# Optimization experiments

Measured on AMD Instinct MI355X. Metric: run time of the kernel, lower is better.

## Reference

```python
import jax, jax.numpy as jnp
import numpy as np
from jax import lax

# BatchNorm2d(affine=False) in eval mode with initial running stats (mean=0, var=1)
# reduces to a constant scale. (Original torch module in train mode would use batch
# stats of the dispatched subset; we use the eval-mode form for a deterministic,
# vectorizable reference.)
BN_SCALE = 1.0 / np.sqrt(1.0 + 1e-5)
DN = ('NCHW', 'OIHW', 'NCHW')


def _dw(x, w, pad, dil=1):
    # depthwise conv, kernel [C,1,k,k]
    return lax.conv_general_dilated(x, w, (1, 1), [(pad, pad), (pad, pad)],
                                    rhs_dilation=(dil, dil), dimension_numbers=DN,
                                    feature_group_count=x.shape[1])


def _pw(x, w):
    # pointwise 1x1 conv, kernel [C,C,1,1]
    return lax.conv_general_dilated(x, w, (1, 1), 'VALID', dimension_numbers=DN)


def _sep(x, d1, p1, d2, p2, pad):
    # DARTS SepConv: (ReLU-dw-pw-BN) x 2
    y = _pw(_dw(jax.nn.relu(x), d1, pad), p1) * BN_SCALE
    return _pw(_dw(jax.nn.relu(y), d2, pad), p2) * BN_SCALE


def _dil(x, d, p, pad):
    # DARTS DilConv: ReLU-dw(dilation=2)-pw-BN
    return _pw(_dw(jax.nn.relu(x), d, pad, 2), p) * BN_SCALE


def _maxpool3(x):
    y = jnp.pad(x, ((0, 0), (0, 0), (1, 1), (1, 1)), constant_values=-jnp.inf)
    return lax.reduce_window(y, -jnp.inf, lax.max, (1, 1, 3, 3), (1, 1, 1, 1), 'VALID')


def _avgpool3(x):
    # avg_pool 3x3 stride 1 pad 1, count_include_pad=False
    pad = [(0, 0), (0, 0), (1, 1), (1, 1)]
    s = lax.reduce_window(x, 0.0, lax.add, (1, 1, 3, 3), (1, 1, 1, 1), pad)
    c = lax.reduce_window(jnp.ones_like(x), 0.0, lax.add, (1, 1, 3, 3), (1, 1, 1, 1), pad)
    return s / c


def _mixed_forward(x, weights, params, top):
    B, n_op = weights.shape
    _, idx = lax.top_k(weights, top)                    # [B, top]
    sel = jax.nn.one_hot(idx, n_op).sum(axis=1) > 0     # [B, n_op] bool: op in top-k
    # softmax over logits masked to -inf outside top-k => non-selected ops weight 0
    gate = jax.nn.softmax(jnp.where(sel, weights, -jnp.inf), axis=-1)  # [B, n_op]
    (sc3_d1, sc3_p1, sc3_d2, sc3_p2,
     sc5_d1, sc5_p1, sc5_d2, sc5_p2,
     dc3_d, dc3_p, dc5_d, dc5_p) = params
    # PRIMITIVES order: none, max_pool_3x3, avg_pool_3x3, skip_connect,
    # sep_conv_3x3, sep_conv_5x5, dil_conv_3x3, dil_conv_5x5
    op_outs = [
        None,                        # 'none' contributes zeros
        _maxpool3(x) * BN_SCALE,     # pool ops are followed by BN(affine=False)
        _avgpool3(x) * BN_SCALE,
        x,                           # skip_connect (stride=1 -> Identity)
        _sep(x, sc3_d1, sc3_p1, sc3_d2, sc3_p2, 1),
        _sep(x, sc5_d1, sc5_p1, sc5_d2, sc5_p2, 2),
        _dil(x, dc3_d, dc3_p, 2),
        _dil(x, dc5_d, dc5_p, 4),
    ]
    out = jnp.zeros_like(x)
    for i, y in enumerate(op_outs):
        if y is not None:
            out = out + gate[:, i, None, None, None] * y
    return out, weights  # second output is gate_value_cp (clone of gate input)


def setup_inputs():
    key = jax.random.key(0)
    ks = jax.random.split(key, 16)
    B, C, H, W = 64, 128, 32, 32
    def p(k, shape):
        return jax.random.normal(k, shape, jnp.float32) * 0.05
    return {
        'x': jax.random.normal(ks[0], (B, C, H, W), jnp.float32),
        'weights': jax.random.normal(ks[1], (B, 8), jnp.float32),
        'sc3_d1': p(ks[2], (C, 1, 3, 3)), 'sc3_p1': p(ks[3], (C, C, 1, 1)),
        'sc3_d2': p(ks[4], (C, 1, 3, 3)), 'sc3_p2': p(ks[5], (C, C, 1, 1)),
        'sc5_d1': p(ks[6], (C, 1, 5, 5)), 'sc5_p1': p(ks[7], (C, C, 1, 1)),
        'sc5_d2': p(ks[8], (C, 1, 5, 5)), 'sc5_p2': p(ks[9], (C, C, 1, 1)),
        'dc3_d': p(ks[10], (C, 1, 3, 3)), 'dc3_p': p(ks[11], (C, C, 1, 1)),
        'dc5_d': p(ks[12], (C, 1, 5, 5)), 'dc5_p': p(ks[13], (C, C, 1, 1)),
        'top': 2,
    }


def reference(x, weights, sc3_d1, sc3_p1, sc3_d2, sc3_p2, sc5_d1, sc5_p1, sc5_d2, sc5_p2, dc3_d, dc3_p, dc5_d, dc5_p, top):
    params = (sc3_d1, sc3_p1, sc3_d2, sc3_p2, sc5_d1, sc5_p1, sc5_d2, sc5_p2,
              dc3_d, dc3_p, dc5_d, dc5_p)
    return _mixed_forward(x, weights, params, top)
```

## Files before the change

### kernel.cpp

```cpp
#include <hip/hip_runtime.h>
#include <hip/hip_bf16.h>


#define BN_SCALE 0.9999950000374997f
#define BB 64
#define CC 128
#define HH 32
#define WW 32
#define PLANE (HH*WW)
#define SAMP (CC*PLANE)
#define NOUT0 (BB*SAMP)

typedef __attribute__((ext_vector_type(8))) short bf16x8;
typedef __attribute__((ext_vector_type(4))) float f32x4;

__device__ __forceinline__ float us2f(unsigned int u) {
    unsigned int x = (u & 0xffffu) << 16;
    float f; __builtin_memcpy(&f, &x, 4); return f;
}
__device__ __forceinline__ unsigned short f2us(float f) {
    __hip_bfloat16 h = __float2bfloat16(f);
    unsigned short u; __builtin_memcpy(&u, &h, 2); return u;
}

__global__ void k_gates(const float* __restrict__ wlog,
                        const void* __restrict__ topp,
                        float* __restrict__ gates,
                        int* __restrict__ cnum, int* __restrict__ cops,
                        float* __restrict__ out_w) {
    int b = threadIdx.x;

    int top = -1;
    {
        unsigned int u0 = *(const unsigned int*)topp;
        int i32 = (int)u0;
        if (i32 >= 1 && i32 <= 8) top = i32;
        else {
            float f32; __builtin_memcpy(&f32, &u0, 4);
            if (f32 >= 1.f && f32 <= 8.f) top = (int)(f32 + 0.5f);
            else { float fb = us2f(u0); if (fb >= 1.f && fb <= 8.f) top = (int)(fb + 0.5f); }
        }
        if (top < 1 || top > 8) top = 2;
    }

    float lw[8];
    #pragma unroll
    for (int i = 0; i < 8; ++i) {
        lw[i] = wlog[b * 8 + i];
        out_w[b * 8 + i] = lw[i];
    }
    bool sel[8] = {false,false,false,false,false,false,false,false};
    for (int t = 0; t < top; ++t) {
        int best = -1; float bv = -3.4e38f;
        #pragma unroll
        for (int i = 0; i < 8; ++i)
            if (!sel[i] && lw[i] > bv) { bv = lw[i]; best = i; }
        if (best >= 0) sel[best] = true;
    }
    float m = -3.4e38f;
    #pragma unroll
    for (int i = 0; i < 8; ++i) if (sel[i] && lw[i] > m) m = lw[i];
    float s = 0.f, e[8];
    #pragma unroll
    for (int i = 0; i < 8; ++i) { e[i] = sel[i] ? expf(lw[i] - m) : 0.f; s += e[i]; }
    float inv = (s > 0.f) ? 1.f / s : 0.f;
    float g[8];
    #pragma unroll
    for (int i = 0; i < 8; ++i) {
        g[i] = (s > 0.f) ? e[i] * inv : (sel[i] ? 1.f / (float)top : 0.f);
        gates[b * 8 + i] = g[i];
    }
    int n = 0;
    #pragma unroll
    for (int i = 4; i < 8; ++i)
        if (g[i] > 0.f) { if (n < 4) cops[b * 4 + n] = i; ++n; }
    cnum[b] = (n < 4) ? n : 4;
}

__global__ __launch_bounds__(256) void
k_prep(const float* __restrict__ w0, const float* __restrict__ w1,
       const float* __restrict__ w2, const float* __restrict__ w3,
       const float* __restrict__ w4, const float* __restrict__ w5,
       unsigned short* __restrict__ Wbf) {
    int idx = blockIdx.x * 256 + threadIdx.x;
    int mat = idx >> 14, e = idx & 16383;
    const float* src; float s = 1.f;
    switch (mat) {
        case 0:  src = w0; s = BN_SCALE; break;
        case 1:  src = w1; s = BN_SCALE; break;
        case 2:  src = w2; break;
        case 3:  src = w3; break;
        case 4:  src = w4; break;
        default: src = w5; break;
    }
    Wbf[idx] = f2us(src[e] * s);
}

__global__ __launch_bounds__(256) void
k_pools(const float* __restrict__ x,
        const float* __restrict__ gates,
        float* __restrict__ out) {
    int plane = blockIdx.x;
    int b = plane >> 7;
    float g1 = gates[b * 8 + 1] * BN_SCALE;
    float g2 = gates[b * 8 + 2] * BN_SCALE;
    float g3 = gates[b * 8 + 3];
    float* op = out + (size_t)plane * PLANE;
    if (g1 == 0.f && g2 == 0.f && g3 == 0.f) {
        ((float4*)op)[threadIdx.x] = make_float4(0.f, 0.f, 0.f, 0.f);
        return;
    }
    __shared__ float sx[PLANE];
    ((float4*)sx)[threadIdx.x] = ((const float4*)(x + (size_t)plane * PLANE))[threadIdx.x];
    __syncthreads();
    #pragma unroll
    for (int j = 0; j < 4; ++j) {
        int px = threadIdx.x + j * 256;
        int h = px >> 5, w = px & 31;
        float mx = -3.4e38f, sm = 0.f;
        int cnt = 0;
        #pragma unroll
        for (int dh = -1; dh <= 1; ++dh) {
            int ih = h + dh;
            if ((unsigned)ih >= HH) continue;
            #pragma unroll
            for (int dw = -1; dw <= 1; ++dw) {
                int iw = w + dw;
                if ((unsigned)iw >= WW) continue;
                float v = sx[ih * WW + iw];
                mx = fmaxf(mx, v);
                sm += v;
                ++cnt;
            }
        }
        op[px] = g1 * mx + g2 * (sm / (float)cnt) + g3 * sx[px];
    }
}

template <int K, int DIL>
__device__ __forceinline__ void dw_comp(const float* __restrict__ sx,
                                        const float* __restrict__ wd, int c,
                                        unsigned short* __restrict__ opp) {
    constexpr int PAD = (K / 2) * DIL;
    float wk[K * K];
    #pragma unroll
    for (int i = 0; i < K * K; ++i) wk[i] = wd[c * K * K + i];
    #pragma unroll
    for (int j = 0; j < 4; ++j) {
        int px = threadIdx.x + j * 256;
        int h = px >> 5, w = px & 31;
        float acc = 0.f;
        #pragma unroll
        for (int ky = 0; ky < K; ++ky) {
            int ih = h + ky * DIL - PAD;
            if ((unsigned)ih >= HH) continue;
            #pragma unroll
            for (int kx = 0; kx < K; ++kx) {
                int iw = w + kx * DIL - PAD;
                if ((unsigned)iw >= WW) continue;
                acc = fmaf(wk[ky * K + kx], sx[ih * WW + iw], acc);
            }
        }
        opp[px] = f2us(acc);
    }
}

__global__ __launch_bounds__(256) void
k_dw_first(const float* __restrict__ x,
           const float* __restrict__ w4, const float* __restrict__ w5,
           const float* __restrict__ w6, const float* __restrict__ w7,
           const float* __restrict__ gates,
           unsigned short* __restrict__ A4, unsigned short* __restrict__ A5,
           unsigned short* __restrict__ P6, unsigned short* __restrict__ P7) {
    int plane = blockIdx.x;
    int b = plane >> 7, c = plane & 127;
    float g4 = gates[b * 8 + 4], g5 = gates[b * 8 + 5];
    float g6 = gates[b * 8 + 6], g7 = gates[b * 8 + 7];
    if (g4 == 0.f && g5 == 0.f && g6 == 0.f && g7 == 0.f) return;
    __shared__ float sx[PLANE];
    {
        float4 v = ((const float4*)(x + (size_t)plane * PLANE))[threadIdx.x];
        ((float4*)sx)[threadIdx.x] =
            make_float4(fmaxf(v.x, 0.f), fmaxf(v.y, 0.f),
                        fmaxf(v.z, 0.f), fmaxf(v.w, 0.f));
    }
    __syncthreads();
    size_t off = (size_t)plane * PLANE;
    if (g4 != 0.f) dw_comp<3, 1>(sx, w4, c, A4 + off);
    if (g5 != 0.f) dw_comp<5, 1>(sx, w5, c, A5 + off);
    if (g6 != 0.f) dw_comp<3, 2>(sx, w6, c, P6 + off);
    if (g7 != 0.f) dw_comp<5, 2>(sx, w7, c, P7 + off);
}

__global__ __launch_bounds__(256) void
k_dw_second(const unsigned short* __restrict__ B4,
            const unsigned short* __restrict__ B5,
            const float* __restrict__ w4, const float* __restrict__ w5,
            const float* __restrict__ gates,
            unsigned short* __restrict__ P4, unsigned short* __restrict__ P5) {
    int plane = blockIdx.x;
    int b = plane >> 7, c = plane & 127;
    float g4 = gates[b * 8 + 4], g5 = gates[b * 8 + 5];
    if (g4 == 0.f && g5 == 0.f) return;
    __shared__ float sx[PLANE];
    size_t off = (size_t)plane * PLANE;
    if (g4 != 0.f) {
        ushort4 v = ((const ushort4*)(B4 + off))[threadIdx.x];
        ((float4*)sx)[threadIdx.x] =
            make_float4(fmaxf(us2f(v.x), 0.f), fmaxf(us2f(v.y), 0.f),
                        fmaxf(us2f(v.z), 0.f), fmaxf(us2f(v.w), 0.f));
        __syncthreads();
        dw_comp<3, 1>(sx, w4, c, P4 + off);
        __syncthreads();
    }
    if (g5 != 0.f) {
        ushort4 v = ((const ushort4*)(B5 + off))[threadIdx.x];
        ((float4*)sx)[threadIdx.x] =
            make_float4(fmaxf(us2f(v.x), 0.f), fmaxf(us2f(v.y), 0.f),
                        fmaxf(us2f(v.z), 0.f), fmaxf(us2f(v.w), 0.f));
        __syncthreads();
        dw_comp<5, 1>(sx, w5, c, P5 + off);
    }
}


__device__ __forceinline__ void stage_bt(unsigned int* __restrict__ BtU,
                                         const unsigned short* __restrict__ A,
                                         int hw0, float s) {
    unsigned short* Bs = (unsigned short*)BtU;
    #pragma unroll
    for (int i = 0; i < 16; ++i) {
        int idx = threadIdx.x + i * 256;
        int ci = idx >> 5, p = idx & 31;
        unsigned int raw = *(const unsigned int*)(A + (size_t)ci * PLANE + hw0 + 2 * p);
        Bs[(2 * p) * 130 + ci]     = f2us(us2f(raw) * s);
        Bs[(2 * p + 1) * 130 + ci] = f2us(us2f(raw >> 16) * s);
    }
}

__device__ __forceinline__ bf16x8 afrag(const unsigned int* __restrict__ BtU,
                                        int r, int ko2) {
    union { unsigned int u[4]; bf16x8 v; } f;
    #pragma unroll
    for (int j = 0; j < 4; ++j) f.u[j] = BtU[r * 65 + ko2 + j];
    return f.v;
}

__global__ __launch_bounds__(256) void
k_pw_mid(const unsigned short* __restrict__ A4,
         const unsigned short* __restrict__ A5,
         const unsigned short* __restrict__ Wbf,
         const float* __restrict__ gates,
         unsigned short* __restrict__ B4, unsigned short* __restrict__ B5) {
    int blk = blockIdx.x;
    int hwt = blk & 15;
    int opi = (blk >> 4) & 1;
    int b = blk >> 5;
    if (gates[b * 8 + 4 + opi] == 0.f) return;
    int hw0 = hwt * 64;
    int wave = threadIdx.x >> 6, lane = threadIdx.x & 63;
    int q = lane >> 4, mm = lane & 15;
    int r = wave * 16 + mm;
    __shared__ unsigned int BtU[64 * 65];
    stage_bt(BtU, (opi ? A5 : A4) + (size_t)b * SAMP, hw0, 1.f);
    __syncthreads();
    const unsigned short* Wb = Wbf + opi * 16384;
    f32x4 acc[8];
    #pragma unroll
    for (int i = 0; i < 8; ++i) acc[i] = (f32x4){0.f, 0.f, 0.f, 0.f};
    #pragma unroll
    for (int kb = 0; kb < 4; ++kb) {
        bf16x8 a = afrag(BtU, r, kb * 16 + q * 4);
        #pragma unroll
        for (int nt = 0; nt < 8; ++nt) {
            bf16x8 bv = *(const bf16x8*)(Wb + (nt * 16 + mm) * CC + kb * 32 + q * 8);
            acc[nt] = __builtin_amdgcn_mfma_f32_16x16x32_bf16(a, bv, acc[nt], 0, 0, 0);
        }
    }
    unsigned short* ob = (opi ? B5 : B4) + (size_t)b * SAMP;
    int hwbase = hw0 + wave * 16 + q * 4;
    #pragma unroll
    for (int nt = 0; nt < 8; ++nt) {
        int co = nt * 16 + mm;
        uint2 pk;
        pk.x = (unsigned int)f2us(acc[nt][0]) | ((unsigned int)f2us(acc[nt][1]) << 16);
        pk.y = (unsigned int)f2us(acc[nt][2]) | ((unsigned int)f2us(acc[nt][3]) << 16);
        *(uint2*)(ob + (size_t)co * PLANE + hwbase) = pk;
    }
}

__global__ __launch_bounds__(256) void
k_pw_final(const unsigned short* __restrict__ P4,
           const unsigned short* __restrict__ P5,
           const unsigned short* __restrict__ P6,
           const unsigned short* __restrict__ P7,
           const unsigned short* __restrict__ Wbf,
           const float* __restrict__ gates,
           const int* __restrict__ cnum, const int* __restrict__ cops,
           float* __restrict__ out) {
    int blk = blockIdx.x;
    int hwt = blk & 15;
    int b = blk >> 4;
    int n = cnum[b];
    if (n == 0) return;
    int hw0 = hwt * 64;
    int wave = threadIdx.x >> 6, lane = threadIdx.x & 63;
    int q = lane >> 4, mm = lane & 15;
    int r = wave * 16 + mm;
    __shared__ unsigned int BtU[64 * 65];
    f32x4 acc[8];
    #pragma unroll
    for (int i = 0; i < 8; ++i) acc[i] = (f32x4){0.f, 0.f, 0.f, 0.f};
    for (int t = 0; t < n; ++t) {
        int op = cops[b * 4 + t];
        float gs = gates[b * 8 + op] * BN_SCALE;
        const unsigned short* src;
        switch (op) {
            case 4:  src = P4; break;
            case 5:  src = P5; break;
            case 6:  src = P6; break;
            default: src = P7; break;
        }
        if (t) __syncthreads();
        stage_bt(BtU, src + (size_t)b * SAMP, hw0, gs);
        __syncthreads();
        const unsigned short* Wb = Wbf + (op - 2) * 16384;
        #pragma unroll
        for (int kb = 0; kb < 4; ++kb) {
            bf16x8 a = afrag(BtU, r, kb * 16 + q * 4);
            #pragma unroll
            for (int nt = 0; nt < 8; ++nt) {
                bf16x8 bv = *(const bf16x8*)(Wb + (nt * 16 + mm) * CC + kb * 32 + q * 8);
                acc[nt] = __builtin_amdgcn_mfma_f32_16x16x32_bf16(a, bv, acc[nt], 0, 0, 0);
            }
        }
    }
    int hwbase = hw0 + wave * 16 + q * 4;
    #pragma unroll
    for (int nt = 0; nt < 8; ++nt) {
        int co = nt * 16 + mm;
        float* p = out + (size_t)(b * CC + co) * PLANE + hwbase;
        float4 o = *(float4*)p;
        o.x += acc[nt][0]; o.y += acc[nt][1];
        o.z += acc[nt][2]; o.w += acc[nt][3];
        *(float4*)p = o;
    }
}

extern "C" void kernel_launch(void* const* d_in, const int* in_sizes, int n_in,
                              void* d_out, int out_size, void* d_ws, size_t ws_size,
                              hipStream_t stream) {
    const float* x      = (const float*)d_in[0];
    const float* wlog   = (const float*)d_in[1];
    const float* sc3_d1 = (const float*)d_in[2];
    const float* sc3_p1 = (const float*)d_in[3];
    const float* sc3_d2 = (const float*)d_in[4];
    const float* sc3_p2 = (const float*)d_in[5];
    const float* sc5_d1 = (const float*)d_in[6];
    const float* sc5_p1 = (const float*)d_in[7];
    const float* sc5_d2 = (const float*)d_in[8];
    const float* sc5_p2 = (const float*)d_in[9];
    const float* dc3_d  = (const float*)d_in[10];
    const float* dc3_p  = (const float*)d_in[11];
    const float* dc5_d  = (const float*)d_in[12];
    const float* dc5_p  = (const float*)d_in[13];
    const void* topp    = d_in[14];

    float* out  = (float*)d_out;
    float* outw = out + NOUT0;

    float* gates = (float*)d_ws;
    int*   cnum  = (int*)((char*)d_ws + 2048);
    int*   cops  = (int*)((char*)d_ws + 2304);
    unsigned short* Wbf  = (unsigned short*)((char*)d_ws + 4096);
    unsigned short* base = (unsigned short*)((char*)d_ws + 200704);
    unsigned short* A4 = base;
    unsigned short* A5 = base + (size_t)NOUT0;
    unsigned short* B4 = base + (size_t)NOUT0 * 2;
    unsigned short* B5 = base + (size_t)NOUT0 * 3;
    unsigned short* P4 = base + (size_t)NOUT0 * 4;
    unsigned short* P5 = base + (size_t)NOUT0 * 5;
    unsigned short* P6 = base + (size_t)NOUT0 * 6;
    unsigned short* P7 = base + (size_t)NOUT0 * 7;

    k_gates<<<1, 64, 0, stream>>>(wlog, topp, gates, cnum, cops, outw);
    k_prep<<<384, 256, 0, stream>>>(sc3_p1, sc5_p1, sc3_p2, sc5_p2, dc3_p, dc5_p, Wbf);
    k_pools<<<BB * CC, 256, 0, stream>>>(x, gates, out);
    k_dw_first<<<BB * CC, 256, 0, stream>>>(x, sc3_d1, sc5_d1, dc3_d, dc5_d,
                                            gates, A4, A5, P6, P7);
    k_pw_mid<<<BB * 32, 256, 0, stream>>>(A4, A5, Wbf, gates, B4, B5);
    k_dw_second<<<BB * CC, 256, 0, stream>>>(B4, B5, sc3_d2, sc5_d2, gates, P4, P5);
    k_pw_final<<<BB * 16, 256, 0, stream>>>(P4, P5, P6, P7, Wbf,
                                            gates, cnum, cops, out);
}
```

Measured before the change: 202.6 us.

## Fuse gates with weight prep and pooling with first depthwise pass

```diff
diff --git a/kernel.cpp b/kernel.cpp
--- a/kernel.cpp
+++ b/kernel.cpp
@@ -23,11 +23,32 @@
     unsigned short u; __builtin_memcpy(&u, &h, 2); return u;
 }
 
-__global__ void k_gates(const float* __restrict__ wlog,
-                        const void* __restrict__ topp,
-                        float* __restrict__ gates,
-                        int* __restrict__ cnum, int* __restrict__ cops,
-                        float* __restrict__ out_w) {
+__global__ __launch_bounds__(256) void
+k_gates_prep(const float* __restrict__ wlog,
+             const void* __restrict__ topp,
+             const float* __restrict__ w0, const float* __restrict__ w1,
+             const float* __restrict__ w2, const float* __restrict__ w3,
+             const float* __restrict__ w4, const float* __restrict__ w5,
+             float* __restrict__ gates,
+             int* __restrict__ cnum, int* __restrict__ cops,
+             float* __restrict__ out_w,
+             unsigned short* __restrict__ Wbf) {
+    if (blockIdx.x != 0) {
+        int idx = (blockIdx.x - 1) * 256 + threadIdx.x;
+        int mat = idx >> 14, e = idx & 16383;
+        const float* src; float s = 1.f;
+        switch (mat) {
+            case 0:  src = w0; s = BN_SCALE; break;
+            case 1:  src = w1; s = BN_SCALE; break;
+            case 2:  src = w2; break;
+            case 3:  src = w3; break;
+            case 4:  src = w4; break;
+            default: src = w5; break;
+        }
+        Wbf[idx] = f2us(src[e] * s);
+        return;
+    }
+    if (threadIdx.x >= BB) return;
     int b = threadIdx.x;
 
     int top = -1;
@@ -77,66 +98,6 @@
     cnum[b] = (n < 4) ? n : 4;
 }
 
-__global__ __launch_bounds__(256) void
-k_prep(const float* __restrict__ w0, const float* __restrict__ w1,
-       const float* __restrict__ w2, const float* __restrict__ w3,
-       const float* __restrict__ w4, const float* __restrict__ w5,
-       unsigned short* __restrict__ Wbf) {
-    int idx = blockIdx.x * 256 + threadIdx.x;
-    int mat = idx >> 14, e = idx & 16383;
-    const float* src; float s = 1.f;
-    switch (mat) {
-        case 0:  src = w0; s = BN_SCALE; break;
-        case 1:  src = w1; s = BN_SCALE; break;
-        case 2:  src = w2; break;
-        case 3:  src = w3; break;
-        case 4:  src = w4; break;
-        default: src = w5; break;
-    }
-    Wbf[idx] = f2us(src[e] * s);
-}
-
-__global__ __launch_bounds__(256) void
-k_pools(const float* __restrict__ x,
-        const float* __restrict__ gates,
-        float* __restrict__ out) {
-    int plane = blockIdx.x;
-    int b = plane >> 7;
-    float g1 = gates[b * 8 + 1] * BN_SCALE;
-    float g2 = gates[b * 8 + 2] * BN_SCALE;
-    float g3 = gates[b * 8 + 3];
-    float* op = out + (size_t)plane * PLANE;
-    if (g1 == 0.f && g2 == 0.f && g3 == 0.f) {
-        ((float4*)op)[threadIdx.x] = make_float4(0.f, 0.f, 0.f, 0.f);
-        return;
-    }
-    __shared__ float sx[PLANE];
-    ((float4*)sx)[threadIdx.x] = ((const float4*)(x + (size_t)plane * PLANE))[threadIdx.x];
-    __syncthreads();
-    #pragma unroll
-    for (int j = 0; j < 4; ++j) {
-        int px = threadIdx.x + j * 256;
-        int h = px >> 5, w = px & 31;
-        float mx = -3.4e38f, sm = 0.f;
-        int cnt = 0;
-        #pragma unroll
-        for (int dh = -1; dh <= 1; ++dh) {
-            int ih = h + dh;
-            if ((unsigned)ih >= HH) continue;
-            #pragma unroll
-            for (int dw = -1; dw <= 1; ++dw) {
-                int iw = w + dw;
-                if ((unsigned)iw >= WW) continue;
-                float v = sx[ih * WW + iw];
-                mx = fmaxf(mx, v);
-                sm += v;
-                ++cnt;
-            }
-        }
-        op[px] = g1 * mx + g2 * (sm / (float)cnt) + g3 * sx[px];
-    }
-}
-
 template <int K, int DIL>
 __device__ __forceinline__ void dw_comp(const float* __restrict__ sx,
                                         const float* __restrict__ wd, int c,
@@ -166,30 +127,70 @@
 }
 
 __global__ __launch_bounds__(256) void
-k_dw_first(const float* __restrict__ x,
-           const float* __restrict__ w4, const float* __restrict__ w5,
-           const float* __restrict__ w6, const float* __restrict__ w7,
-           const float* __restrict__ gates,
-           unsigned short* __restrict__ A4, unsigned short* __restrict__ A5,
-           unsigned short* __restrict__ P6, unsigned short* __restrict__ P7) {
+k_front(const float* __restrict__ x,
+        const float* __restrict__ w4, const float* __restrict__ w5,
+        const float* __restrict__ w6, const float* __restrict__ w7,
+        const float* __restrict__ gates,
+        float* __restrict__ out,
+        unsigned short* __restrict__ A4, unsigned short* __restrict__ A5,
+        unsigned short* __restrict__ P6, unsigned short* __restrict__ P7) {
     int plane = blockIdx.x;
     int b = plane >> 7, c = plane & 127;
+    float g1 = gates[b * 8 + 1] * BN_SCALE;
+    float g2 = gates[b * 8 + 2] * BN_SCALE;
+    float g3 = gates[b * 8 + 3];
     float g4 = gates[b * 8 + 4], g5 = gates[b * 8 + 5];
     float g6 = gates[b * 8 + 6], g7 = gates[b * 8 + 7];
-    if (g4 == 0.f && g5 == 0.f && g6 == 0.f && g7 == 0.f) return;
-    __shared__ float sx[PLANE];
+    bool haspool = (g1 != 0.f) | (g2 != 0.f) | (g3 != 0.f);
+    bool hasdw   = (g4 != 0.f) | (g5 != 0.f) | (g6 != 0.f) | (g7 != 0.f);
+    float* op = out + (size_t)plane * PLANE;
+    if (!haspool && !hasdw) {
+        ((float4*)op)[threadIdx.x] = make_float4(0.f, 0.f, 0.f, 0.f);
+        return;
+    }
+    __shared__ float sxr[PLANE];
+    __shared__ float sxf[PLANE];
     {
         float4 v = ((const float4*)(x + (size_t)plane * PLANE))[threadIdx.x];
-        ((float4*)sx)[threadIdx.x] =
+        ((float4*)sxr)[threadIdx.x] = v;
+        ((float4*)sxf)[threadIdx.x] =
             make_float4(fmaxf(v.x, 0.f), fmaxf(v.y, 0.f),
                         fmaxf(v.z, 0.f), fmaxf(v.w, 0.f));
     }
     __syncthreads();
+
+    if (haspool) {
+        #pragma unroll
+        for (int j = 0; j < 4; ++j) {
+            int px = threadIdx.x + j * 256;
+            int h = px >> 5, w = px & 31;
+            float mx = -3.4e38f, sm = 0.f;
+            int cnt = 0;
+            #pragma unroll
+            for (int dh = -1; dh <= 1; ++dh) {
+                int ih = h + dh;
+                if ((unsigned)ih >= HH) continue;
+                #pragma unroll
+                for (int dw = -1; dw <= 1; ++dw) {
+                    int iw = w + dw;
+                    if ((unsigned)iw >= WW) continue;
+                    float v = sxr[ih * WW + iw];
+                    mx = fmaxf(mx, v);
+                    sm += v;
+                    ++cnt;
+                }
+            }
+            op[px] = g1 * mx + g2 * (sm / (float)cnt) + g3 * sxr[px];
+        }
+    } else {
+        ((float4*)op)[threadIdx.x] = make_float4(0.f, 0.f, 0.f, 0.f);
+    }
+
     size_t off = (size_t)plane * PLANE;
-    if (g4 != 0.f) dw_comp<3, 1>(sx, w4, c, A4 + off);
-    if (g5 != 0.f) dw_comp<5, 1>(sx, w5, c, A5 + off);
-    if (g6 != 0.f) dw_comp<3, 2>(sx, w6, c, P6 + off);
-    if (g7 != 0.f) dw_comp<5, 2>(sx, w7, c, P7 + off);
+    if (g4 != 0.f) dw_comp<3, 1>(sxf, w4, c, A4 + off);
+    if (g5 != 0.f) dw_comp<5, 1>(sxf, w5, c, A5 + off);
+    if (g6 != 0.f) dw_comp<3, 2>(sxf, w6, c, P6 + off);
+    if (g7 != 0.f) dw_comp<5, 2>(sxf, w7, c, P7 + off);
 }
 
 __global__ __launch_bounds__(256) void
@@ -383,11 +384,12 @@
     unsigned short* P6 = base + (size_t)NOUT0 * 6;
     unsigned short* P7 = base + (size_t)NOUT0 * 7;
 
-    k_gates<<<1, 64, 0, stream>>>(wlog, topp, gates, cnum, cops, outw);
-    k_prep<<<384, 256, 0, stream>>>(sc3_p1, sc5_p1, sc3_p2, sc5_p2, dc3_p, dc5_p, Wbf);
-    k_pools<<<BB * CC, 256, 0, stream>>>(x, gates, out);
-    k_dw_first<<<BB * CC, 256, 0, stream>>>(x, sc3_d1, sc5_d1, dc3_d, dc5_d,
-                                            gates, A4, A5, P6, P7);
+    k_gates_prep<<<385, 256, 0, stream>>>(wlog, topp,
+                                          sc3_p1, sc5_p1, sc3_p2, sc5_p2,
+                                          dc3_p, dc5_p,
+                                          gates, cnum, cops, outw, Wbf);
+    k_front<<<BB * CC, 256, 0, stream>>>(x, sc3_d1, sc5_d1, dc3_d, dc5_d,
+                                         gates, out, A4, A5, P6, P7);
     k_pw_mid<<<BB * 32, 256, 0, stream>>>(A4, A5, Wbf, gates, B4, B5);
     k_dw_second<<<BB * CC, 256, 0, stream>>>(B4, B5, sc3_d2, sc5_d2, gates, P4, P5);
     k_pw_final<<<BB * 16, 256, 0, stream>>>(P4, P5, P6, P7, Wbf,
```

Result: faster. 191.9 us (-5.3%).
